# Optimization experiments

Hardware: AMD Instinct MI355X
Metric: run time of the kernel (lower is better)

Reference implementation:

```python
import jax, jax.numpy as jnp
import numpy as np

N_NODES, N_EDGES, WIDTH = 50000, 640000, 128


def setup_inputs() -> dict:
    key = jax.random.key(0)
    k1, k2, k3 = jax.random.split(key, 3)
    x = jax.random.normal(k1, (N_NODES, WIDTH), dtype=jnp.float32)
    e = jax.random.randint(k2, (2, N_EDGES), 0, N_NODES, dtype=jnp.int32)
    # LinearBlock(2*width, width): Linear(256 -> 128) + ReLU
    W = jax.random.normal(k3, (WIDTH, 2 * WIDTH), dtype=jnp.float32) * (1.0 / np.sqrt(2 * WIDTH))
    b = jnp.zeros((WIDTH,), dtype=jnp.float32)
    return {"x": x, "e": e, "W": W, "b": b}


def reference(x, e, W, b):
    src, dst = e[0], e[1]
    # gather-subtract: diffs[k] = x[dst_k] - x[src_k]  -> [E, width]
    diffs = x[dst] - x[src]
    n = x.shape[0]
    # scatter_max over destination nodes; torch_scatter leaves empty segments at 0
    maxes = jax.ops.segment_max(diffs, dst, num_segments=n)  # [N, width]
    deg = jax.ops.segment_sum(jnp.ones((dst.shape[0],), jnp.float32), dst, num_segments=n)
    maxes = jnp.where((deg > 0)[:, None], maxes, 0.0)
    # LinearBlock (Linear + ReLU) on concat, then residual
    h = jnp.concatenate([x, maxes], axis=1)  # [N, 2*width]
    return x + jax.nn.relu(h @ W.T + b)
```

## Files before the change

### kernel.cpp

```cpp
#include <hip/hip_runtime.h>
#include <hip/hip_bf16.h>

#define WIDTH   128
#define NNODES  50000
#define NEDGES  640000
#define NTILES  3125
#define TILES_PER_BLOCK 4
#define WLDS_STRIDE 264
#define CAP     64

typedef __attribute__((ext_vector_type(8))) short  short8;
typedef __attribute__((ext_vector_type(4))) short  short4_t;
typedef __attribute__((ext_vector_type(4))) float  float4_t;

__device__ inline short f2bf(float f) {
    union { float f; unsigned int u; } a;
    a.f = f;
    unsigned int r = a.u + 0x7FFFu + ((a.u >> 16) & 1u);
    return (short)(r >> 16);
}
__device__ inline unsigned int pack2bf(float a, float b) {
    unsigned int lo = (unsigned short)f2bf(a);
    unsigned int hi = (unsigned short)f2bf(b);
    return lo | (hi << 16);
}
__device__ inline float bflo(unsigned int u) { return __uint_as_float(u << 16); }
__device__ inline float bfhi(unsigned int u) { return __uint_as_float(u & 0xFFFF0000u); }

__global__ __launch_bounds__(256) void convert_zero_kernel(
    const float* __restrict__ x, uint2* __restrict__ xb2, int* __restrict__ counts)
{
    int i = blockIdx.x * 256 + threadIdx.x;
    float4 v = *(const float4*)(x + (size_t)i * 4);
    uint2 p;
    p.x = pack2bf(v.x, v.y);
    p.y = pack2bf(v.z, v.w);
    xb2[i] = p;
    if (i < 16384) *(int4*)(counts + i * 4) = make_int4(0, 0, 0, 0);
}

__global__ __launch_bounds__(256) void fill_kernel(
    const int* __restrict__ e, int* __restrict__ counts, int* __restrict__ buckets)
{
    int i = blockIdx.x * 256 + threadIdx.x;
    if (i >= NEDGES) return;
    int src = e[i];
    int dst = e[NEDGES + i];
    int pos = atomicAdd(&counts[dst], 1);
    if (pos < CAP) buckets[dst * CAP + pos] = src;
}

__global__ __launch_bounds__(256) void gather_min_bf16_kernel(
    const uint2* __restrict__ xb2, const int* __restrict__ counts,
    const int* __restrict__ buckets, uint2* __restrict__ maxes2)
{
    int wave = (blockIdx.x * 256 + threadIdx.x) >> 6;
    int lane = threadIdx.x & 63;
    if (wave >= NNODES) return;
    int node = wave;
    int deg  = counts[node];
    deg = deg > CAP ? CAP : deg;

    int myidx = (lane < deg) ? buckets[node * CAP + lane] : 0;
    int h  = lane >> 5;
    int cl = lane & 31;

    float4 m; m.x = 3.4e38f; m.y = 3.4e38f; m.z = 3.4e38f; m.w = 3.4e38f;
#pragma unroll 1
    for (int j0 = 0; j0 < deg; j0 += 16) {
        uint2 v[8];
#pragma unroll
        for (int u = 0; u < 8; ++u) {
            int jc = j0 + 2 * u + h;
            jc = jc < deg ? jc : deg - 1;
            int src = __shfl(myidx, jc);
            v[u] = xb2[(size_t)src * 32 + cl];
        }
#pragma unroll
        for (int u = 0; u < 8; ++u) {
            m.x = fminf(m.x, bflo(v[u].x));
            m.y = fminf(m.y, bfhi(v[u].x));
            m.z = fminf(m.z, bflo(v[u].y));
            m.w = fminf(m.w, bfhi(v[u].y));
        }
    }
    m.x = fminf(m.x, __shfl_xor(m.x, 32));
    m.y = fminf(m.y, __shfl_xor(m.y, 32));
    m.z = fminf(m.z, __shfl_xor(m.z, 32));
    m.w = fminf(m.w, __shfl_xor(m.w, 32));

    if (h == 0) {
        uint2 o;
        if (deg > 0) {
            uint2 xv = xb2[(size_t)node * 32 + cl];
            o.x = pack2bf(bflo(xv.x) - m.x, bfhi(xv.x) - m.y);
            o.y = pack2bf(bflo(xv.y) - m.z, bfhi(xv.y) - m.w);
        } else {
            o.x = 0u; o.y = 0u;
        }
        maxes2[(size_t)node * 32 + cl] = o;
    }
}

__global__ __launch_bounds__(256) void gather_min_fp32_kernel(
    const float* __restrict__ x, const int* __restrict__ counts,
    const int* __restrict__ buckets, unsigned int* __restrict__ maxes_u32)
{
    int wave = (blockIdx.x * 256 + threadIdx.x) >> 6;
    int lane = threadIdx.x & 63;
    if (wave >= NNODES) return;
    int node = wave;
    int deg  = counts[node];
    deg = deg > CAP ? CAP : deg;

    int myidx = (lane < deg) ? buckets[node * CAP + lane] : 0;
    int c = lane * 2;
    float2 m; m.x = 3.4e38f; m.y = 3.4e38f;
#pragma unroll 1
    for (int j0 = 0; j0 < deg; j0 += 8) {
        float2 v[8];
#pragma unroll
        for (int u = 0; u < 8; ++u) {
            int jc = j0 + u;
            jc = jc < deg ? jc : deg - 1;
            int src = __shfl(myidx, jc);
            v[u] = *(const float2*)(x + (size_t)src * WIDTH + c);
        }
#pragma unroll
        for (int u = 0; u < 8; ++u) {
            m.x = fminf(m.x, v[u].x);
            m.y = fminf(m.y, v[u].y);
        }
    }
    float2 o;
    if (deg > 0) {
        float2 xv = *(const float2*)(x + (size_t)node * WIDTH + c);
        o.x = xv.x - m.x;
        o.y = xv.y - m.y;
    } else { o.x = 0.f; o.y = 0.f; }
    maxes_u32[(size_t)node * 64 + lane] = pack2bf(o.x, o.y);
}

template<bool XB>
__global__ __launch_bounds__(256, 2) void fused_gemm_kernel(
    const float* __restrict__ x, const short* __restrict__ xb,
    const short* __restrict__ maxes,
    const float* __restrict__ W, const float* __restrict__ b,
    float* __restrict__ out)
{
    __shared__ short Wlds[WIDTH * WLDS_STRIDE];

    const int t = threadIdx.x;

#pragma unroll
    for (int i = 0; i < 32; ++i) {
        int idx4 = t + i * 256;
        int flat = idx4 << 2;
        float4 w = *(const float4*)(W + flat);
        int n = flat >> 8;
        int k = flat & 255;
        short4_t s;
        s.x = f2bf(w.x); s.y = f2bf(w.y); s.z = f2bf(w.z); s.w = f2bf(w.w);
        *(short4_t*)&Wlds[n * WLDS_STRIDE + k] = s;
    }
    __syncthreads();

    const int wave  = t >> 6;
    const int lane  = t & 63;
    const int lm    = lane & 15;
    const int quad  = lane >> 4;
    const int nhalf = wave & 1;
    const int wpair = wave >> 1;
    const int ncol_base = nhalf * 64;

    short8 bfrag[4][8];
#pragma unroll
    for (int nt = 0; nt < 4; ++nt) {
        int n = ncol_base + nt * 16 + lm;
#pragma unroll
        for (int kt = 0; kt < 8; ++kt) {
            int k = kt * 32 + quad * 8;
            bfrag[nt][kt] = *(const short8*)&Wlds[n * WLDS_STRIDE + k];
        }
    }

    const int tile0 = blockIdx.x * TILES_PER_BLOCK;
#pragma unroll 1
    for (int i = 0; i < TILES_PER_BLOCK / 2; ++i) {
        int tile = tile0 + 2 * i + wpair;
        if (tile >= NTILES) break;
        int row = tile * 16 + lm;
        const float* xr  = x     + (size_t)row * WIDTH;
        const short* xbr = XB ? (xb + (size_t)row * WIDTH) : nullptr;
        const short* mr  = maxes + (size_t)row * WIDTH;

        float4_t acc[4];
#pragma unroll
        for (int nt = 0; nt < 4; ++nt) { acc[nt].x = 0.f; acc[nt].y = 0.f; acc[nt].z = 0.f; acc[nt].w = 0.f; }

#pragma unroll
        for (int kt = 0; kt < 8; ++kt) {
            int k = kt * 32 + quad * 8;
            short8 afrag;
            if (k < WIDTH) {
                if (XB) {
                    afrag = *(const short8*)(xbr + k);
                } else {
                    float4 v0 = *(const float4*)(xr + k);
                    float4 v1 = *(const float4*)(xr + k + 4);
                    afrag[0] = f2bf(v0.x); afrag[1] = f2bf(v0.y);
                    afrag[2] = f2bf(v0.z); afrag[3] = f2bf(v0.w);
                    afrag[4] = f2bf(v1.x); afrag[5] = f2bf(v1.y);
                    afrag[6] = f2bf(v1.z); afrag[7] = f2bf(v1.w);
                }
            } else {
                afrag = *(const short8*)(mr + (k - WIDTH));
            }
#pragma unroll
            for (int nt = 0; nt < 4; ++nt) {
                acc[nt] = __builtin_amdgcn_mfma_f32_16x16x32_bf16(
                    afrag, bfrag[nt][kt], acc[nt], 0, 0, 0);
            }
        }

#pragma unroll
        for (int nt = 0; nt < 4; ++nt) {
            int col = ncol_base + nt * 16 + lm;
            float bias = b[col];
#pragma unroll
            for (int r = 0; r < 4; ++r) {
                int orow = tile * 16 + quad * 4 + r;
                float v = acc[nt][r] + bias;
                v = v > 0.f ? v : 0.f;
                size_t off = (size_t)orow * WIDTH + col;
                out[off] = x[off] + v;
            }
        }
    }
}

extern "C" void kernel_launch(void* const* d_in, const int* in_sizes, int n_in,
                              void* d_out, int out_size, void* d_ws, size_t ws_size,
                              hipStream_t stream) {
    const float* x = (const float*)d_in[0];
    const int*   e = (const int*)  d_in[1];
    const float* W = (const float*)d_in[2];
    const float* b = (const float*)d_in[3];
    float* out = (float*)d_out;

    char* ws = (char*)d_ws;
    int*          counts  = (int*)ws;
    int*          buckets = (int*)(ws + 262144);
    unsigned int* maxes   = (unsigned int*)(ws + 262144 + 12800000);
    short*        xb      = (short*)(ws + 262144 + 2 * 12800000);

    const size_t need_xb = 262144 + 3ull * 12800000;
    const bool use_xb = (ws_size >= need_xb);

    int gemm_blocks = (NTILES + TILES_PER_BLOCK - 1) / TILES_PER_BLOCK;

    if (use_xb) {
        convert_zero_kernel<<<6250, 256, 0, stream>>>(x, (uint2*)xb, counts);
        fill_kernel<<<(NEDGES + 255) / 256, 256, 0, stream>>>(e, counts, buckets);
        gather_min_bf16_kernel<<<(NNODES + 3) / 4, 256, 0, stream>>>(
            (const uint2*)xb, counts, buckets, (uint2*)maxes);
        fused_gemm_kernel<true><<<gemm_blocks, 256, 0, stream>>>(
            x, xb, (const short*)maxes, W, b, out);
    } else {
        hipMemsetAsync(counts, 0, 262144, stream);
        fill_kernel<<<(NEDGES + 255) / 256, 256, 0, stream>>>(e, counts, buckets);
        gather_min_fp32_kernel<<<(NNODES + 3) / 4, 256, 0, stream>>>(
            x, counts, buckets, maxes);
        fused_gemm_kernel<false><<<gemm_blocks, 256, 0, stream>>>(
            x, nullptr, (const short*)maxes, W, b, out);
    }
}
```

Measured before the change: 161.2 us.

## Replace global-atomic edge bucketing with LDS-binned per-segment buckets

Swaps the global-atomic fill of per-destination buckets for a binning kernel. Each block owns a node range and an edge segment, counts with LDS atomics, and writes into per-segment bucket slots, which also removes the need to zero the counts buffer. The gather kernel then compacts the eight segment slots with ballot/mbcnt and ds_permute into a contiguous index list. The aim is to avoid contended global atomics. In exchange, every block scans a whole edge segment (edges are read 32 times), the bucket buffer doubles in size, and per-segment capacity is capped at 16, which could drop edges for high-degree nodes.

Measured after the change: 283.4 us. +75.8%, slower.

```diff
diff --git a/kernel.cpp b/kernel.cpp
--- a/kernel.cpp
+++ b/kernel.cpp
@@ -7,7 +7,13 @@
 #define NTILES  3125
 #define TILES_PER_BLOCK 4
 #define WLDS_STRIDE 264
-#define CAP     64
+
+#define RBLK    32
+#define SSEG    8
+#define RSZ     1563
+#define SEG_EDGES 80000
+#define C0      16
+#define CAPB    128
 
 typedef __attribute__((ext_vector_type(8))) short  short8;
 typedef __attribute__((ext_vector_type(4))) short  short4_t;
@@ -27,8 +33,8 @@
 __device__ inline float bflo(unsigned int u) { return __uint_as_float(u << 16); }
 __device__ inline float bfhi(unsigned int u) { return __uint_as_float(u & 0xFFFF0000u); }
 
-__global__ __launch_bounds__(256) void convert_zero_kernel(
-    const float* __restrict__ x, uint2* __restrict__ xb2, int* __restrict__ counts)
+__global__ __launch_bounds__(256) void convert_kernel(
+    const float* __restrict__ x, uint2* __restrict__ xb2)
 {
     int i = blockIdx.x * 256 + threadIdx.x;
     float4 v = *(const float4*)(x + (size_t)i * 4);
@@ -36,32 +42,70 @@
     p.x = pack2bf(v.x, v.y);
     p.y = pack2bf(v.z, v.w);
     xb2[i] = p;
-    if (i < 16384) *(int4*)(counts + i * 4) = make_int4(0, 0, 0, 0);
-}
-
-__global__ __launch_bounds__(256) void fill_kernel(
-    const int* __restrict__ e, int* __restrict__ counts, int* __restrict__ buckets)
-{
-    int i = blockIdx.x * 256 + threadIdx.x;
-    if (i >= NEDGES) return;
-    int src = e[i];
-    int dst = e[NEDGES + i];
-    int pos = atomicAdd(&counts[dst], 1);
-    if (pos < CAP) buckets[dst * CAP + pos] = src;
+}
+
+__global__ __launch_bounds__(256) void bin_kernel(
+    const int* __restrict__ e, int* __restrict__ counts2, int* __restrict__ buckets)
+{
+    __shared__ int cnt[RSZ];
+    int r = blockIdx.x & (RBLK - 1);
+    int s = blockIdx.x / RBLK;
+    int base = r * RSZ;
+    int rsz  = NNODES - base; if (rsz > RSZ) rsz = RSZ;
+
+    for (int i = threadIdx.x; i < RSZ; i += 256) cnt[i] = 0;
+    __syncthreads();
+
+    int e0 = s * SEG_EDGES, e1 = e0 + SEG_EDGES;
+    for (int i = e0 + threadIdx.x; i < e1; i += 256) {
+        int dst = e[NEDGES + i];
+        unsigned d = (unsigned)(dst - base);
+        if (d < (unsigned)rsz) {
+            int pos = atomicAdd(&cnt[d], 1);
+            if (pos < C0) {
+                int src = e[i];
+                buckets[dst * CAPB + s * C0 + pos] = src;
+            }
+        }
+    }
+    __syncthreads();
+    for (int i = threadIdx.x; i < rsz; i += 256) {
+        int c = cnt[i]; if (c > C0) c = C0;
+        counts2[(base + i) * SSEG + s] = c;
+    }
 }
 
 __global__ __launch_bounds__(256) void gather_min_bf16_kernel(
-    const uint2* __restrict__ xb2, const int* __restrict__ counts,
+    const uint2* __restrict__ xb2, const int* __restrict__ counts2,
     const int* __restrict__ buckets, uint2* __restrict__ maxes2)
 {
     int wave = (blockIdx.x * 256 + threadIdx.x) >> 6;
     int lane = threadIdx.x & 63;
     if (wave >= NNODES) return;
     int node = wave;
-    int deg  = counts[node];
-    deg = deg > CAP ? CAP : deg;
-
-    int myidx = (lane < deg) ? buckets[node * CAP + lane] : 0;
+
+    int s0 = lane >> 4;
+    int j  = lane & 15;
+    int c0 = counts2[node * SSEG + s0];
+    int c1 = counts2[node * SSEG + 4 + s0];
+    int idx0 = buckets[node * CAPB + lane];
+    int idx1 = buckets[node * CAPB + 64 + lane];
+    bool v0 = j < c0;
+    bool v1 = j < c1;
+    unsigned long long m0 = __ballot(v0);
+    unsigned long long m1 = __ballot(v1);
+    int p0 = __builtin_amdgcn_mbcnt_hi((unsigned)(m0 >> 32),
+             __builtin_amdgcn_mbcnt_lo((unsigned)m0, 0));
+    int popc0 = __popcll(m0);
+    int p1 = popc0 + __builtin_amdgcn_mbcnt_hi((unsigned)(m1 >> 32),
+                     __builtin_amdgcn_mbcnt_lo((unsigned)m1, 0));
+    int deg = popc0 + __popcll(m1);
+    int t0 = v0 ? p0 : 63;
+    int t1 = v1 ? p1 : 63;
+    int r0 = __builtin_amdgcn_ds_permute(t0 << 2, idx0);
+    int r1 = __builtin_amdgcn_ds_permute(t1 << 2, idx1);
+    int myidx = (lane < popc0) ? r0 : r1;
+
     int h  = lane >> 5;
     int cl = lane & 31;
 
@@ -102,6 +146,17 @@
     }
 }
 
+__global__ __launch_bounds__(256) void fill_kernel(
+    const int* __restrict__ e, int* __restrict__ counts, int* __restrict__ buckets)
+{
+    int i = blockIdx.x * 256 + threadIdx.x;
+    if (i >= NEDGES) return;
+    int src = e[i];
+    int dst = e[NEDGES + i];
+    int pos = atomicAdd(&counts[dst], 1);
+    if (pos < 64) buckets[dst * 64 + pos] = src;
+}
+
 __global__ __launch_bounds__(256) void gather_min_fp32_kernel(
     const float* __restrict__ x, const int* __restrict__ counts,
     const int* __restrict__ buckets, unsigned int* __restrict__ maxes_u32)
@@ -111,9 +166,9 @@
     if (wave >= NNODES) return;
     int node = wave;
     int deg  = counts[node];
-    deg = deg > CAP ? CAP : deg;
-
-    int myidx = (lane < deg) ? buckets[node * CAP + lane] : 0;
+    deg = deg > 64 ? 64 : deg;
+
+    int myidx = (lane < deg) ? buckets[node * 64 + lane] : 0;
     int c = lane * 2;
     float2 m; m.x = 3.4e38f; m.y = 3.4e38f;
 #pragma unroll 1
@@ -249,24 +304,30 @@
     float* out = (float*)d_out;
 
     char* ws = (char*)d_ws;
-    int*          counts  = (int*)ws;
-    int*          buckets = (int*)(ws + 262144);
-    unsigned int* maxes   = (unsigned int*)(ws + 262144 + 12800000);
-    short*        xb      = (short*)(ws + 262144 + 2 * 12800000);
-
-    const size_t need_xb = 262144 + 3ull * 12800000;
-    const bool use_xb = (ws_size >= need_xb);
-
     int gemm_blocks = (NTILES + TILES_PER_BLOCK - 1) / TILES_PER_BLOCK;
 
-    if (use_xb) {
-        convert_zero_kernel<<<6250, 256, 0, stream>>>(x, (uint2*)xb, counts);
-        fill_kernel<<<(NEDGES + 255) / 256, 256, 0, stream>>>(e, counts, buckets);
+    const size_t off_buckets = 1600000;
+    const size_t off_maxes   = off_buckets + (size_t)NNODES * CAPB * 4;
+    const size_t off_xb      = off_maxes + 12800000;
+    const size_t need        = off_xb + 12800000;
+
+    if (ws_size >= need) {
+        int*          counts2 = (int*)ws;
+        int*          buckets = (int*)(ws + off_buckets);
+        unsigned int* maxes   = (unsigned int*)(ws + off_maxes);
+        short*        xb      = (short*)(ws + off_xb);
+
+        convert_kernel<<<6250, 256, 0, stream>>>(x, (uint2*)xb);
+        bin_kernel<<<RBLK * SSEG, 256, 0, stream>>>(e, counts2, buckets);
         gather_min_bf16_kernel<<<(NNODES + 3) / 4, 256, 0, stream>>>(
-            (const uint2*)xb, counts, buckets, (uint2*)maxes);
+            (const uint2*)xb, counts2, buckets, (uint2*)maxes);
         fused_gemm_kernel<true><<<gemm_blocks, 256, 0, stream>>>(
             x, xb, (const short*)maxes, W, b, out);
     } else {
+        int*          counts  = (int*)ws;
+        int*          buckets = (int*)(ws + 262144);
+        unsigned int* maxes   = (unsigned int*)(ws + 262144 + 12800000);
+
         hipMemsetAsync(counts, 0, 262144, stream);
         fill_kernel<<<(NEDGES + 255) / 256, 256, 0, stream>>>(e, counts, buckets);
         gather_min_fp32_kernel<<<(NNODES + 3) / 4, 256, 0, stream>>>(
```
